# Kernel optimization log

Hardware: AMD Instinct MI355X
Metric: run time of the kernel (lower is better)

Reference implementation:

```python
import jax, jax.numpy as jnp
import numpy as np

B, NL, NT = 8, 64, 512   # graphs, ligand atoms/graph, target nodes/graph
CF = 128                 # per-node embedding dim (Linear(256,...) => 2*128)
H = 128                  # hidden_dim
K = 10                   # n_gaussians
E = 1024                 # ligand edges
BN_EPS = 1e-4


def setup_inputs() -> dict:
    key = jax.random.key(0)
    ks = jax.random.split(key, 24)
    inp = {}
    inp["h_l_x"] = jax.random.normal(ks[0], (B * NL, CF), jnp.float32)
    inp["h_t_x"] = jax.random.normal(ks[1], (B * NT, CF), jnp.float32)
    inp["h_l_pos"] = jax.random.normal(ks[2], (B * NL, 3), jnp.float32)
    inp["h_t_pos"] = jax.random.normal(ks[3], (B * NT, 3), jnp.float32)
    inp["edge_index"] = jax.random.randint(ks[4], (2, E), 0, B * NL, jnp.int64)
    s = 0.05
    inp["W1"] = jax.random.normal(ks[5], (2 * CF, H), jnp.float32) * s
    inp["b1"] = jnp.zeros((H,), jnp.float32)
    inp["gamma"] = jnp.ones((H,), jnp.float32)
    inp["beta"] = jnp.zeros((H,), jnp.float32)
    inp["rmean"] = jax.random.normal(ks[6], (H,), jnp.float32) * 0.1
    inp["rvar"] = jax.random.uniform(ks[7], (H,), jnp.float32, 0.5, 1.5)
    inp["Wpi"] = jax.random.normal(ks[8], (H, K), jnp.float32) * s
    inp["bpi"] = jnp.zeros((K,), jnp.float32)
    inp["Wsig"] = jax.random.normal(ks[9], (H, K), jnp.float32) * s
    inp["bsig"] = jnp.zeros((K,), jnp.float32)
    inp["Wmu"] = jax.random.normal(ks[10], (H, K), jnp.float32) * s
    inp["bmu"] = jnp.zeros((K,), jnp.float32)
    inp["Wat"] = jax.random.normal(ks[11], (CF, 28), jnp.float32) * s
    inp["bat"] = jnp.zeros((28,), jnp.float32)
    inp["Wbd"] = jax.random.normal(ks[12], (2 * CF, 6), jnp.float32) * s
    inp["bbd"] = jnp.zeros((6,), jnp.float32)
    return inp


def reference(h_l_x, h_t_x, h_l_pos, h_t_pos, edge_index,
              W1, b1, gamma, beta, rmean, rvar,
              Wpi, bpi, Wsig, bsig, Wmu, bmu, Wat, bat, Wbd, bbd):
    # dense batched node features (equal counts per graph => reshape)
    hl = h_l_x.reshape(B, NL, CF)
    ht = h_t_x.reshape(B, NT, CF)

    # cat([hl_repeat, ht_repeat]) @ W1 == hl@W1[:CF] + ht@W1[CF:] (broadcast add)
    zl = jnp.einsum('blc,ch->blh', hl, W1[:CF])          # [B,NL,H]
    zt = jnp.einsum('btc,ch->bth', ht, W1[CF:])          # [B,NT,H]
    z = zl[:, :, None, :] + zt[:, None, :, :] + b1       # [B,NL,NT,H]
    z = z.reshape(B * NL * NT, H)

    # BatchNorm1d (eval: running stats), ELU; Dropout is identity in eval
    z = (z - rmean) * (gamma / jnp.sqrt(rvar + BN_EPS)) + beta
    C = jax.nn.elu(z)

    pi = jax.nn.softmax(C @ Wpi + bpi, axis=-1)
    sigma = jax.nn.elu(C @ Wsig + bsig) + 1.1
    mu = jax.nn.elu(C @ Wmu + bmu) + 1.0

    # pairwise euclidean distances, detached in original
    pl = h_l_pos.reshape(B, NL, 3)
    pt = h_t_pos.reshape(B, NT, 3)
    d2 = (-2.0 * jnp.einsum('bld,btd->blt', pl, pt)
          + jnp.sum(pt ** 2, -1)[:, None, :]
          + jnp.sum(pl ** 2, -1)[:, :, None])
    dist = jnp.sqrt(d2).reshape(B * NL * NT)
    dist = jax.lax.stop_gradient(dist)[:, None]          # [P,1]

    atom_types = h_l_x @ Wat + bat                       # [B*NL,28]
    eb = jnp.concatenate([h_l_x[edge_index[0]], h_l_x[edge_index[1]]], axis=1)
    bond_types = eb @ Wbd + bbd                          # [E,6]

    C_batch = jnp.repeat(jnp.arange(B, dtype=jnp.int32), NL * NT)
    return (pi, sigma, mu, dist, atom_types, bond_types, C_batch)
```

## Files before the change

kernel.cpp:

```cpp
#include <hip/hip_runtime.h>
#include <hip/hip_bf16.h>
#include <cstdint>
#include <cstddef>

#define NB_B 8
#define NL   64
#define NT   512
#define CF   128
#define HD   128
#define NK   10
#define NE   1024

static constexpr size_t P_TOT    = (size_t)NB_B * NL * NT;
static constexpr size_t PI_OFF   = 0;
static constexpr size_t SIG_OFF  = P_TOT * 10;
static constexpr size_t MU_OFF   = SIG_OFF + P_TOT * 10;
static constexpr size_t DIST_OFF = MU_OFF + P_TOT * 10;
static constexpr size_t AT_OFF   = DIST_OFF + P_TOT;
static constexpr size_t BD_OFF   = AT_OFF + 512 * 28;
static constexpr size_t CB_OFF   = BD_OFF + NE * 6;

typedef __attribute__((ext_vector_type(8))) short short8;
typedef __attribute__((ext_vector_type(4))) float floatx4;
typedef __attribute__((ext_vector_type(2))) float floatx2;

union U8 { short8 s8; unsigned int u[4]; };

__device__ __forceinline__ float bf2f(unsigned short u) {
    return __uint_as_float(((unsigned int)u) << 16);
}
__device__ __forceinline__ unsigned short f2bf(float f) {
    unsigned int x = __float_as_uint(f);
    x = (x + 0x7FFFu + ((x >> 16) & 1u)) >> 16;
    return (unsigned short)x;
}
__device__ __forceinline__ unsigned int pk2bf(float a, float b) {
    __hip_bfloat162 h = __float22bfloat162_rn(make_float2(a, b));
    return *reinterpret_cast<unsigned int*>(&h);
}
__device__ __forceinline__ float elu(float x) {
    return fmaxf(x, 0.f) + (__expf(fminf(x, 0.f)) - 1.f);
}

__global__ __launch_bounds__(256) void k_pre(
    const float* __restrict__ hl,
    const float* __restrict__ ht,
    const float* __restrict__ W1,
    const float* __restrict__ b1,
    const float* __restrict__ gamma_,
    const float* __restrict__ beta_,
    const float* __restrict__ rmean,
    const float* __restrict__ rvar,
    const float* __restrict__ Wpi,
    const float* __restrict__ Wsig,
    const float* __restrict__ Wmu,
    unsigned short* __restrict__ zl,
    unsigned short* __restrict__ zt,
    unsigned short* __restrict__ wcomb_t)
{
    const int blk = blockIdx.x;
    const int tid = threadIdx.x;

    if (blk < 144) {
        const bool is_l = (blk < 16);
        const int rbase = is_l ? blk * 32 : (blk - 16) * 32;
        const float* A  = is_l ? hl : ht;
        const float* Wx = W1 + (is_l ? 0 : (size_t)CF * HD);
        unsigned short* Z = is_l ? zl : zt;

        const int wave = tid >> 6;
        const int lane = tid & 63;
        const int m    = lane & 15;
        const int kq   = (lane >> 4) * 8;
        const int n0   = wave * 32 + m;

        floatx4 acc[2][2];
        #pragma unroll
        for (int i = 0; i < 2; ++i)
            #pragma unroll
            for (int j = 0; j < 2; ++j)
                acc[i][j] = (floatx4){0.f, 0.f, 0.f, 0.f};

        #pragma unroll
        for (int kb = 0; kb < 4; ++kb) {
            const int k0 = kb * 32 + kq;
            short8 a[2];
            #pragma unroll
            for (int mt = 0; mt < 2; ++mt) {
                const float* ap = A + (size_t)(rbase + mt * 16 + m) * CF + k0;
                const float4 f0 = *(const float4*)ap;
                const float4 f1 = *(const float4*)(ap + 4);
                U8 t;
                t.u[0] = pk2bf(f0.x, f0.y);
                t.u[1] = pk2bf(f0.z, f0.w);
                t.u[2] = pk2bf(f1.x, f1.y);
                t.u[3] = pk2bf(f1.z, f1.w);
                a[mt] = t.s8;
            }
            short8 bf[2];
            #pragma unroll
            for (int nt = 0; nt < 2; ++nt) {
                const int n = n0 + nt * 16;
                float w[8];
                #pragma unroll
                for (int j = 0; j < 8; ++j)
                    w[j] = Wx[(size_t)(k0 + j) * HD + n];
                U8 t;
                #pragma unroll
                for (int j = 0; j < 4; ++j) t.u[j] = pk2bf(w[2*j], w[2*j+1]);
                bf[nt] = t.s8;
            }
            #pragma unroll
            for (int mt = 0; mt < 2; ++mt)
                #pragma unroll
                for (int nt = 0; nt < 2; ++nt)
                    acc[mt][nt] = __builtin_amdgcn_mfma_f32_16x16x32_bf16(a[mt], bf[nt], acc[mt][nt], 0, 0, 0);
        }

        #pragma unroll
        for (int nt = 0; nt < 2; ++nt) {
            const int col = n0 + nt * 16;
            const float s   = gamma_[col] * rsqrtf(rvar[col] + 1e-4f);
            const float off = is_l ? 0.f : ((b1[col] - rmean[col]) * s + beta_[col]);
            #pragma unroll
            for (int mt = 0; mt < 2; ++mt)
                #pragma unroll
                for (int r = 0; r < 4; ++r) {
                    const int row = rbase + mt * 16 + (lane >> 4) * 4 + r;
                    Z[(size_t)row * HD + col] = f2bf(acc[mt][nt][r] * s + off);
                }
        }
    } else {
        for (int i = tid; i < 32 * HD; i += 256) {
            const int n = i >> 7, k = i & 127;
            float v = 0.f;
            if (n < 10)      v = Wpi [k * NK + n];
            else if (n < 20) v = Wsig[k * NK + (n - 10)];
            else if (n < 30) v = Wmu [k * NK + (n - 20)];
            wcomb_t[i] = f2bf(v);
        }
    }
}

__global__ __launch_bounds__(256) void k_main(
    const unsigned short* __restrict__ zl,
    const unsigned short* __restrict__ zt,
    const unsigned short* __restrict__ wcomb_t,
    const float* __restrict__ bpi,
    const float* __restrict__ bsig,
    const float* __restrict__ bmu,
    const float* __restrict__ hlpos,
    const float* __restrict__ htpos,
    const float* __restrict__ hl,
    const int*   __restrict__ eidx,
    const float* __restrict__ Wat,
    const float* __restrict__ bat,
    const float* __restrict__ Wbd,
    const float* __restrict__ bbd,
    float* __restrict__ out)
{
    __shared__ float Dl[128 * 34];
    __shared__ float biass[32];
    __shared__ float pls[3];

    const int tid  = threadIdx.x;
    const int blk  = blockIdx.x;
    const int lane = tid & 63;
    const int wave = tid >> 6;
    const int m    = lane & 15;
    const int quad = lane >> 4;

    if (blk >= 2048) {
        const int ab = blk - 2048;
        if (ab < 4) {
            const int rbase = ab * 128 + wave * 32;
            floatx4 acc[2][2];
            #pragma unroll
            for (int i = 0; i < 2; ++i)
                #pragma unroll
                for (int j = 0; j < 2; ++j)
                    acc[i][j] = (floatx4){0.f, 0.f, 0.f, 0.f};
            #pragma unroll
            for (int kb = 0; kb < 4; ++kb) {
                const int k0 = kb * 32 + quad * 8;
                short8 a[2];
                #pragma unroll
                for (int mt = 0; mt < 2; ++mt) {
                    const float* ap = hl + (size_t)(rbase + mt * 16 + m) * CF + k0;
                    const float4 f0 = *(const float4*)ap;
                    const float4 f1 = *(const float4*)(ap + 4);
                    U8 t;
                    t.u[0] = pk2bf(f0.x, f0.y);
                    t.u[1] = pk2bf(f0.z, f0.w);
                    t.u[2] = pk2bf(f1.x, f1.y);
                    t.u[3] = pk2bf(f1.z, f1.w);
                    a[mt] = t.s8;
                }
                short8 bf[2];
                #pragma unroll
                for (int nt = 0; nt < 2; ++nt) {
                    const int n = nt * 16 + m;
                    const int nc = (n < 28) ? n : 0;
                    #pragma unroll
                    for (int j = 0; j < 8; ++j) {
                        const float w = Wat[(size_t)(k0 + j) * 28 + nc];
                        bf[nt][j] = (short)f2bf((n < 28) ? w : 0.f);
                    }
                }
                #pragma unroll
                for (int mt = 0; mt < 2; ++mt)
                    #pragma unroll
                    for (int nt = 0; nt < 2; ++nt)
                        acc[mt][nt] = __builtin_amdgcn_mfma_f32_16x16x32_bf16(a[mt], bf[nt], acc[mt][nt], 0, 0, 0);
            }
            #pragma unroll
            for (int nt = 0; nt < 2; ++nt) {
                const int col = nt * 16 + m;
                if (col < 28) {
                    const float bias = bat[col];
                    #pragma unroll
                    for (int mt = 0; mt < 2; ++mt)
                        #pragma unroll
                        for (int r = 0; r < 4; ++r) {
                            const int row = rbase + mt * 16 + quad * 4 + r;
                            out[AT_OFF + (size_t)row * 28 + col] = acc[mt][nt][r] + bias;
                        }
                }
            }
        } else {
            const int rbase = (ab - 4) * 128 + wave * 32;
            const int e0 = rbase + m, e1 = rbase + 16 + m;
            const int s00 = eidx[e0], s01 = eidx[NE + e0];
            const int s10 = eidx[e1], s11 = eidx[NE + e1];
            floatx4 acc[2];
            acc[0] = (floatx4){0.f, 0.f, 0.f, 0.f};
            acc[1] = (floatx4){0.f, 0.f, 0.f, 0.f};
            const int nc = (m < 6) ? m : 0;
            #pragma unroll
            for (int kb = 0; kb < 8; ++kb) {
                const int k0 = kb * 32 + quad * 8;
                const bool lo = (k0 < 128);
                const int off = lo ? k0 : (k0 - 128);
                short8 a[2];
                #pragma unroll
                for (int mt = 0; mt < 2; ++mt) {
                    const int src = lo ? (mt ? s10 : s00) : (mt ? s11 : s01);
                    const float* ap = hl + (size_t)src * CF + off;
                    const float4 f0 = *(const float4*)ap;
                    const float4 f1 = *(const float4*)(ap + 4);
                    U8 t;
                    t.u[0] = pk2bf(f0.x, f0.y);
                    t.u[1] = pk2bf(f0.z, f0.w);
                    t.u[2] = pk2bf(f1.x, f1.y);
                    t.u[3] = pk2bf(f1.z, f1.w);
                    a[mt] = t.s8;
                }
                short8 bf;
                #pragma unroll
                for (int j = 0; j < 8; ++j) {
                    const float w = Wbd[(size_t)(k0 + j) * 6 + nc];
                    bf[j] = (short)f2bf((m < 6) ? w : 0.f);
                }
                acc[0] = __builtin_amdgcn_mfma_f32_16x16x32_bf16(a[0], bf, acc[0], 0, 0, 0);
                acc[1] = __builtin_amdgcn_mfma_f32_16x16x32_bf16(a[1], bf, acc[1], 0, 0, 0);
            }
            if (m < 6) {
                const float bias = bbd[m];
                #pragma unroll
                for (int mt = 0; mt < 2; ++mt)
                    #pragma unroll
                    for (int r = 0; r < 4; ++r) {
                        const int row = rbase + mt * 16 + quad * 4 + r;
                        out[BD_OFF + (size_t)row * 6 + m] = acc[mt][r] + bias;
                    }
            }
        }
        return;
    }

    const int b  = blk >> 8;
    const int l  = (blk >> 2) & 63;
    const int ch = blk & 3;

    if (tid < 32) {
        float v = 0.f;
        if (tid < 10)      v = bpi[tid];
        else if (tid < 20) v = bsig[tid - 10];
        else if (tid < 30) v = bmu[tid - 20];
        biass[tid] = v;
    } else if (tid < 35) {
        pls[tid - 32] = hlpos[(size_t)(b * NL + l) * 3 + (tid - 32)];
    }

    short8 bfrag[2][4];
    #pragma unroll
    for (int nt = 0; nt < 2; ++nt)
        #pragma unroll
        for (int kb = 0; kb < 4; ++kb)
            bfrag[nt][kb] = *(const short8*)(wcomb_t + (size_t)(nt * 16 + m) * HD + kb * 32 + quad * 8);

    const unsigned short* zlr = zl + (size_t)(b * NL + l) * HD;
    const unsigned short* ztb = zt + (size_t)(b * NT + ch * 128) * HD;

    floatx4 acc[2][2];
    #pragma unroll
    for (int i = 0; i < 2; ++i)
        #pragma unroll
        for (int j = 0; j < 2; ++j)
            acc[i][j] = (floatx4){0.f, 0.f, 0.f, 0.f};

    #pragma unroll
    for (int kb = 0; kb < 4; ++kb) {
        const int k0 = kb * 32 + quad * 8;
        const short8 zlv = *(const short8*)(zlr + k0);
        float zf[8];
        #pragma unroll
        for (int j = 0; j < 8; ++j) zf[j] = bf2f((unsigned short)zlv[j]);

        short8 a[2];
        #pragma unroll
        for (int mt = 0; mt < 2; ++mt) {
            const int row = wave * 32 + mt * 16 + m;
            const short8 ztv = *(const short8*)(ztb + (size_t)row * HD + k0);
            float e[8];
            #pragma unroll
            for (int j = 0; j < 8; ++j)
                e[j] = elu(zf[j] + bf2f((unsigned short)ztv[j]));
            U8 t;
            #pragma unroll
            for (int j = 0; j < 4; ++j) t.u[j] = pk2bf(e[2*j], e[2*j+1]);
            a[mt] = t.s8;
        }
        #pragma unroll
        for (int mt = 0; mt < 2; ++mt)
            #pragma unroll
            for (int nt = 0; nt < 2; ++nt)
                acc[mt][nt] = __builtin_amdgcn_mfma_f32_16x16x32_bf16(a[mt], bfrag[nt][kb], acc[mt][nt], 0, 0, 0);
    }

    #pragma unroll
    for (int mt = 0; mt < 2; ++mt)
        #pragma unroll
        for (int nt = 0; nt < 2; ++nt)
            #pragma unroll
            for (int r = 0; r < 4; ++r) {
                const int row = wave * 32 + mt * 16 + quad * 4 + r;
                const int col = nt * 16 + m;
                Dl[row * 34 + col] = acc[mt][nt][r];
            }
    __syncthreads();

    const size_t gp = ((size_t)(b * NL + l)) * NT + ch * 128 + (tid & 127);
    if (tid < 128) {
        const int p = tid;
        float v[10];
        float mx = -1e30f;
        #pragma unroll
        for (int n = 0; n < 10; ++n) {
            v[n] = Dl[p * 34 + n] + biass[n];
            mx = fmaxf(mx, v[n]);
        }
        float s = 0.f;
        #pragma unroll
        for (int n = 0; n < 10; ++n) { v[n] = __expf(v[n] - mx); s += v[n]; }
        const float inv = 1.f / s;
        floatx2* po = (floatx2*)(out + PI_OFF + gp * 10);
        #pragma unroll
        for (int n = 0; n < 5; ++n) po[n] = (floatx2){v[2*n] * inv, v[2*n+1] * inv};
    } else {
        const int p = tid - 128;
        float sg[10], mv[10];
        #pragma unroll
        for (int n = 0; n < 10; ++n) {
            sg[n] = elu(Dl[p * 34 + 10 + n] + biass[10 + n]) + 1.1f;
            mv[n] = elu(Dl[p * 34 + 20 + n] + biass[20 + n]) + 1.0f;
        }
        floatx2* ps = (floatx2*)(out + SIG_OFF + gp * 10);
        floatx2* pm = (floatx2*)(out + MU_OFF  + gp * 10);
        #pragma unroll
        for (int n = 0; n < 5; ++n) {
            ps[n] = (floatx2){sg[2*n], sg[2*n+1]};
            pm[n] = (floatx2){mv[2*n], mv[2*n+1]};
        }
        const int t = ch * 128 + p;
        const size_t pb = (size_t)(b * NT + t) * 3;
        const float dx = pls[0] - htpos[pb + 0];
        const float dy = pls[1] - htpos[pb + 1];
        const float dz = pls[2] - htpos[pb + 2];
        out[DIST_OFF + gp] = sqrtf(dx * dx + dy * dy + dz * dz);
        out[CB_OFF + gp]   = (float)b;
    }
}

extern "C" void kernel_launch(void* const* d_in, const int* in_sizes, int n_in,
                              void* d_out, int out_size, void* d_ws, size_t ws_size,
                              hipStream_t stream)
{
    const float* hl     = (const float*)d_in[0];
    const float* ht     = (const float*)d_in[1];
    const float* hlpos  = (const float*)d_in[2];
    const float* htpos  = (const float*)d_in[3];
    const int*   eidx   = (const int*)d_in[4];
    const float* W1     = (const float*)d_in[5];
    const float* b1     = (const float*)d_in[6];
    const float* gamma_ = (const float*)d_in[7];
    const float* beta_  = (const float*)d_in[8];
    const float* rmean  = (const float*)d_in[9];
    const float* rvar   = (const float*)d_in[10];
    const float* Wpi    = (const float*)d_in[11];
    const float* bpi    = (const float*)d_in[12];
    const float* Wsig   = (const float*)d_in[13];
    const float* bsig   = (const float*)d_in[14];
    const float* Wmu    = (const float*)d_in[15];
    const float* bmu    = (const float*)d_in[16];
    const float* Wat    = (const float*)d_in[17];
    const float* bat    = (const float*)d_in[18];
    const float* Wbd    = (const float*)d_in[19];
    const float* bbd    = (const float*)d_in[20];

    float* out = (float*)d_out;
    unsigned short* ws  = (unsigned short*)d_ws;
    unsigned short* zl      = ws;
    unsigned short* zt      = ws + 512 * 128;
    unsigned short* wcomb_t = ws + 512 * 128 + 4096 * 128;

    k_pre<<<145, 256, 0, stream>>>(hl, ht, W1, b1, gamma_, beta_, rmean, rvar,
                                   Wpi, Wsig, Wmu, zl, zt, wcomb_t);
    k_main<<<2060, 256, 0, stream>>>(zl, zt, wcomb_t, bpi, bsig, bmu, hlpos, htpos,
                                     hl, eidx, Wat, bat, Wbd, bbd, out);
}
```

Baseline: 132.3 us.

## Fuse pre and main kernels into one persistent kernel with grid barrier

Merges the projection kernel and the main pairwise kernel into one launch of 1024 blocks. The blocks first compute zl/zt (now 16-row tiles over 288 blocks), meet at an atomic-counter grid barrier, then each block loops over two work units of the former main grid. The aim is to remove the second kernel launch and the gap between the two kernels. In exchange it adds a memset and a spin barrier. The barrier deadlocks unless all 1024 blocks are resident at once, which depends on occupancy (launch_bounds 256,4).

```diff
diff --git a/kernel.cpp b/kernel.cpp
--- a/kernel.cpp
+++ b/kernel.cpp
@@ -10,6 +10,7 @@
 #define HD   128
 #define NK   10
 #define NE   1024
+#define NBLK 1024u
 
 static constexpr size_t P_TOT    = (size_t)NB_B * NL * NT;
 static constexpr size_t PI_OFF   = 0;
@@ -42,9 +43,12 @@
     return fmaxf(x, 0.f) + (__expf(fminf(x, 0.f)) - 1.f);
 }
 
-__global__ __launch_bounds__(256) void k_pre(
+__global__ __launch_bounds__(256, 4) void k_all(
     const float* __restrict__ hl,
     const float* __restrict__ ht,
+    const float* __restrict__ hlpos,
+    const float* __restrict__ htpos,
+    const int*   __restrict__ eidx,
     const float* __restrict__ W1,
     const float* __restrict__ b1,
     const float* __restrict__ gamma_,
@@ -52,51 +56,57 @@
     const float* __restrict__ rmean,
     const float* __restrict__ rvar,
     const float* __restrict__ Wpi,
+    const float* __restrict__ bpi,
     const float* __restrict__ Wsig,
+    const float* __restrict__ bsig,
     const float* __restrict__ Wmu,
+    const float* __restrict__ bmu,
+    const float* __restrict__ Wat,
+    const float* __restrict__ bat,
+    const float* __restrict__ Wbd,
+    const float* __restrict__ bbd,
     unsigned short* __restrict__ zl,
     unsigned short* __restrict__ zt,
-    unsigned short* __restrict__ wcomb_t)
+    unsigned short* __restrict__ wcomb_t,
+    unsigned int*   __restrict__ cnt,
+    float* __restrict__ out)
 {
-    const int blk = blockIdx.x;
-    const int tid = threadIdx.x;
-
-    if (blk < 144) {
-        const bool is_l = (blk < 16);
-        const int rbase = is_l ? blk * 32 : (blk - 16) * 32;
+    __shared__ float Dl[128 * 34];
+    __shared__ float biass[32];
+    __shared__ float pls[3];
+
+    const int blk0 = blockIdx.x;
+    const int tid  = threadIdx.x;
+    const int lane = tid & 63;
+    const int wave = tid >> 6;
+    const int m    = lane & 15;
+    const int quad = lane >> 4;
+
+    if (blk0 < 288) {
+        const bool is_l = (blk0 < 32);
+        const int rbase = is_l ? blk0 * 16 : (blk0 - 32) * 16;
         const float* A  = is_l ? hl : ht;
         const float* Wx = W1 + (is_l ? 0 : (size_t)CF * HD);
         unsigned short* Z = is_l ? zl : zt;
-
-        const int wave = tid >> 6;
-        const int lane = tid & 63;
-        const int m    = lane & 15;
-        const int kq   = (lane >> 4) * 8;
-        const int n0   = wave * 32 + m;
-
-        floatx4 acc[2][2];
-        #pragma unroll
-        for (int i = 0; i < 2; ++i)
-            #pragma unroll
-            for (int j = 0; j < 2; ++j)
-                acc[i][j] = (floatx4){0.f, 0.f, 0.f, 0.f};
+        const int n0 = wave * 32 + m;
+
+        floatx4 acc[2];
+        acc[0] = (floatx4){0.f, 0.f, 0.f, 0.f};
+        acc[1] = (floatx4){0.f, 0.f, 0.f, 0.f};
 
         #pragma unroll
         for (int kb = 0; kb < 4; ++kb) {
-            const int k0 = kb * 32 + kq;
-            short8 a[2];
-            #pragma unroll
-            for (int mt = 0; mt < 2; ++mt) {
-                const float* ap = A + (size_t)(rbase + mt * 16 + m) * CF + k0;
-                const float4 f0 = *(const float4*)ap;
-                const float4 f1 = *(const float4*)(ap + 4);
-                U8 t;
-                t.u[0] = pk2bf(f0.x, f0.y);
-                t.u[1] = pk2bf(f0.z, f0.w);
-                t.u[2] = pk2bf(f1.x, f1.y);
-                t.u[3] = pk2bf(f1.z, f1.w);
-                a[mt] = t.s8;
-            }
+            const int k0 = kb * 32 + quad * 8;
+            const float* ap = A + (size_t)(rbase + m) * CF + k0;
+            const float4 f0 = *(const float4*)ap;
+            const float4 f1 = *(const float4*)(ap + 4);
+            U8 t;
+            t.u[0] = pk2bf(f0.x, f0.y);
+            t.u[1] = pk2bf(f0.z, f0.w);
+            t.u[2] = pk2bf(f1.x, f1.y);
+            t.u[3] = pk2bf(f1.z, f1.w);
+            const short8 a = t.s8;
+
             short8 bf[2];
             #pragma unroll
             for (int nt = 0; nt < 2; ++nt) {
@@ -105,16 +115,14 @@
                 #pragma unroll
                 for (int j = 0; j < 8; ++j)
                     w[j] = Wx[(size_t)(k0 + j) * HD + n];
-                U8 t;
-                #pragma unroll
-                for (int j = 0; j < 4; ++j) t.u[j] = pk2bf(w[2*j], w[2*j+1]);
-                bf[nt] = t.s8;
-            }
-            #pragma unroll
-            for (int mt = 0; mt < 2; ++mt)
-                #pragma unroll
-                for (int nt = 0; nt < 2; ++nt)
-                    acc[mt][nt] = __builtin_amdgcn_mfma_f32_16x16x32_bf16(a[mt], bf[nt], acc[mt][nt], 0, 0, 0);
+                U8 tt;
+                #pragma unroll
+                for (int j = 0; j < 4; ++j) tt.u[j] = pk2bf(w[2*j], w[2*j+1]);
+                bf[nt] = tt.s8;
+            }
+            #pragma unroll
+            for (int nt = 0; nt < 2; ++nt)
+                acc[nt] = __builtin_amdgcn_mfma_f32_16x16x32_bf16(a, bf[nt], acc[nt], 0, 0, 0);
         }
 
         #pragma unroll
@@ -123,14 +131,12 @@
             const float s   = gamma_[col] * rsqrtf(rvar[col] + 1e-4f);
             const float off = is_l ? 0.f : ((b1[col] - rmean[col]) * s + beta_[col]);
             #pragma unroll
-            for (int mt = 0; mt < 2; ++mt)
-                #pragma unroll
-                for (int r = 0; r < 4; ++r) {
-                    const int row = rbase + mt * 16 + (lane >> 4) * 4 + r;
-                    Z[(size_t)row * HD + col] = f2bf(acc[mt][nt][r] * s + off);
-                }
-        }
-    } else {
+            for (int r = 0; r < 4; ++r) {
+                const int row = rbase + quad * 4 + r;
+                Z[(size_t)row * HD + col] = f2bf(acc[nt][r] * s + off);
+            }
+        }
+    } else if (blk0 == 288) {
         for (int i = tid; i < 32 * HD; i += 256) {
             const int n = i >> 7, k = i & 127;
             float v = 0.f;
@@ -140,255 +146,243 @@
             wcomb_t[i] = f2bf(v);
         }
     }
-}
-
-__global__ __launch_bounds__(256) void k_main(
-    const unsigned short* __restrict__ zl,
-    const unsigned short* __restrict__ zt,
-    const unsigned short* __restrict__ wcomb_t,
-    const float* __restrict__ bpi,
-    const float* __restrict__ bsig,
-    const float* __restrict__ bmu,
-    const float* __restrict__ hlpos,
-    const float* __restrict__ htpos,
-    const float* __restrict__ hl,
-    const int*   __restrict__ eidx,
-    const float* __restrict__ Wat,
-    const float* __restrict__ bat,
-    const float* __restrict__ Wbd,
-    const float* __restrict__ bbd,
-    float* __restrict__ out)
-{
-    __shared__ float Dl[128 * 34];
-    __shared__ float biass[32];
-    __shared__ float pls[3];
-
-    const int tid  = threadIdx.x;
-    const int blk  = blockIdx.x;
-    const int lane = tid & 63;
-    const int wave = tid >> 6;
-    const int m    = lane & 15;
-    const int quad = lane >> 4;
-
-    if (blk >= 2048) {
-        const int ab = blk - 2048;
-        if (ab < 4) {
-            const int rbase = ab * 128 + wave * 32;
-            floatx4 acc[2][2];
-            #pragma unroll
-            for (int i = 0; i < 2; ++i)
-                #pragma unroll
-                for (int j = 0; j < 2; ++j)
-                    acc[i][j] = (floatx4){0.f, 0.f, 0.f, 0.f};
-            #pragma unroll
-            for (int kb = 0; kb < 4; ++kb) {
-                const int k0 = kb * 32 + quad * 8;
-                short8 a[2];
-                #pragma unroll
-                for (int mt = 0; mt < 2; ++mt) {
-                    const float* ap = hl + (size_t)(rbase + mt * 16 + m) * CF + k0;
-                    const float4 f0 = *(const float4*)ap;
-                    const float4 f1 = *(const float4*)(ap + 4);
-                    U8 t;
-                    t.u[0] = pk2bf(f0.x, f0.y);
-                    t.u[1] = pk2bf(f0.z, f0.w);
-                    t.u[2] = pk2bf(f1.x, f1.y);
-                    t.u[3] = pk2bf(f1.z, f1.w);
-                    a[mt] = t.s8;
+
+    __threadfence();
+    __syncthreads();
+    if (tid == 0) {
+        __hip_atomic_fetch_add(cnt, 1u, __ATOMIC_ACQ_REL, __HIP_MEMORY_SCOPE_AGENT);
+        unsigned int v;
+        do {
+            v = __hip_atomic_load(cnt, __ATOMIC_ACQUIRE, __HIP_MEMORY_SCOPE_AGENT);
+            if (v >= NBLK) break;
+            __builtin_amdgcn_s_sleep(2);
+        } while (true);
+    }
+    __syncthreads();
+    __threadfence();
+
+    for (int u = blk0; u < 2060; u += 1024) {
+        if (u >= 2048) {
+            const int ab = u - 2048;
+            if (ab < 4) {
+                const int rbase = ab * 128 + wave * 32;
+                floatx4 acc[2][2];
+                #pragma unroll
+                for (int i = 0; i < 2; ++i)
+                    #pragma unroll
+                    for (int j = 0; j < 2; ++j)
+                        acc[i][j] = (floatx4){0.f, 0.f, 0.f, 0.f};
+                #pragma unroll
+                for (int kb = 0; kb < 4; ++kb) {
+                    const int k0 = kb * 32 + quad * 8;
+                    short8 a[2];
+                    #pragma unroll
+                    for (int mt = 0; mt < 2; ++mt) {
+                        const float* ap = hl + (size_t)(rbase + mt * 16 + m) * CF + k0;
+                        const float4 f0 = *(const float4*)ap;
+                        const float4 f1 = *(const float4*)(ap + 4);
+                        U8 t;
+                        t.u[0] = pk2bf(f0.x, f0.y);
+                        t.u[1] = pk2bf(f0.z, f0.w);
+                        t.u[2] = pk2bf(f1.x, f1.y);
+                        t.u[3] = pk2bf(f1.z, f1.w);
+                        a[mt] = t.s8;
+                    }
+                    short8 bf[2];
+                    #pragma unroll
+                    for (int nt = 0; nt < 2; ++nt) {
+                        const int n = nt * 16 + m;
+                        const int nc = (n < 28) ? n : 0;
+                        #pragma unroll
+                        for (int j = 0; j < 8; ++j) {
+                            const float w = Wat[(size_t)(k0 + j) * 28 + nc];
+                            bf[nt][j] = (short)f2bf((n < 28) ? w : 0.f);
+                        }
+                    }
+                    #pragma unroll
+                    for (int mt = 0; mt < 2; ++mt)
+                        #pragma unroll
+                        for (int nt = 0; nt < 2; ++nt)
+                            acc[mt][nt] = __builtin_amdgcn_mfma_f32_16x16x32_bf16(a[mt], bf[nt], acc[mt][nt], 0, 0, 0);
                 }
-                short8 bf[2];
                 #pragma unroll
                 for (int nt = 0; nt < 2; ++nt) {
-                    const int n = nt * 16 + m;
-                    const int nc = (n < 28) ? n : 0;
-                    #pragma unroll
-                    for (int j = 0; j < 8; ++j) {
-                        const float w = Wat[(size_t)(k0 + j) * 28 + nc];
-                        bf[nt][j] = (short)f2bf((n < 28) ? w : 0.f);
+                    const int col = nt * 16 + m;
+                    if (col < 28) {
+                        const float bias = bat[col];
+                        #pragma unroll
+                        for (int mt = 0; mt < 2; ++mt)
+                            #pragma unroll
+                            for (int r = 0; r < 4; ++r) {
+                                const int row = rbase + mt * 16 + quad * 4 + r;
+                                out[AT_OFF + (size_t)row * 28 + col] = acc[mt][nt][r] + bias;
+                            }
                     }
                 }
-                #pragma unroll
-                for (int mt = 0; mt < 2; ++mt)
-                    #pragma unroll
-                    for (int nt = 0; nt < 2; ++nt)
-                        acc[mt][nt] = __builtin_amdgcn_mfma_f32_16x16x32_bf16(a[mt], bf[nt], acc[mt][nt], 0, 0, 0);
-            }
-            #pragma unroll
-            for (int nt = 0; nt < 2; ++nt) {
-                const int col = nt * 16 + m;
-                if (col < 28) {
-                    const float bias = bat[col];
+            } else {
+                const int rbase = (ab - 4) * 128 + wave * 32;
+                const int e0 = rbase + m, e1 = rbase + 16 + m;
+                const int s00 = eidx[e0], s01 = eidx[NE + e0];
+                const int s10 = eidx[e1], s11 = eidx[NE + e1];
+                floatx4 acc[2];
+                acc[0] = (floatx4){0.f, 0.f, 0.f, 0.f};
+                acc[1] = (floatx4){0.f, 0.f, 0.f, 0.f};
+                const int nc = (m < 6) ? m : 0;
+                #pragma unroll
+                for (int kb = 0; kb < 8; ++kb) {
+                    const int k0 = kb * 32 + quad * 8;
+                    const bool lo = (k0 < 128);
+                    const int off = lo ? k0 : (k0 - 128);
+                    short8 a[2];
+                    #pragma unroll
+                    for (int mt = 0; mt < 2; ++mt) {
+                        const int src = lo ? (mt ? s10 : s00) : (mt ? s11 : s01);
+                        const float* ap = hl + (size_t)src * CF + off;
+                        const float4 f0 = *(const float4*)ap;
+                        const float4 f1 = *(const float4*)(ap + 4);
+                        U8 t;
+                        t.u[0] = pk2bf(f0.x, f0.y);
+                        t.u[1] = pk2bf(f0.z, f0.w);
+                        t.u[2] = pk2bf(f1.x, f1.y);
+                        t.u[3] = pk2bf(f1.z, f1.w);
+                        a[mt] = t.s8;
+                    }
+                    short8 bf;
+                    #pragma unroll
+                    for (int j = 0; j < 8; ++j) {
+                        const float w = Wbd[(size_t)(k0 + j) * 6 + nc];
+                        bf[j] = (short)f2bf((m < 6) ? w : 0.f);
+                    }
+                    acc[0] = __builtin_amdgcn_mfma_f32_16x16x32_bf16(a[0], bf, acc[0], 0, 0, 0);
+                    acc[1] = __builtin_amdgcn_mfma_f32_16x16x32_bf16(a[1], bf, acc[1], 0, 0, 0);
+                }
+                if (m < 6) {
+                    const float bias = bbd[m];
                     #pragma unroll
                     for (int mt = 0; mt < 2; ++mt)
                         #pragma unroll
                         for (int r = 0; r < 4; ++r) {
                             const int row = rbase + mt * 16 + quad * 4 + r;
-                            out[AT_OFF + (size_t)row * 28 + col] = acc[mt][nt][r] + bias;
+                            out[BD_OFF + (size_t)row * 6 + m] = acc[mt][r] + bias;
                         }
                 }
             }
+            continue;
+        }
+
+        const int b  = u >> 8;
+        const int l  = (u >> 2) & 63;
+        const int ch = u & 3;
+
+        if (tid < 32) {
+            float v = 0.f;
+            if (tid < 10)      v = bpi[tid];
+            else if (tid < 20) v = bsig[tid - 10];
+            else if (tid < 30) v = bmu[tid - 20];
+            biass[tid] = v;
+        } else if (tid < 35) {
+            pls[tid - 32] = hlpos[(size_t)(b * NL + l) * 3 + (tid - 32)];
+        }
+
+        short8 bfrag[2][4];
+        #pragma unroll
+        for (int nt = 0; nt < 2; ++nt)
+            #pragma unroll
+            for (int kb = 0; kb < 4; ++kb)
+                bfrag[nt][kb] = *(const short8*)(wcomb_t + (size_t)(nt * 16 + m) * HD + kb * 32 + quad * 8);
+
+        const unsigned short* zlr = zl + (size_t)(b * NL + l) * HD;
+        const unsigned short* ztb = zt + (size_t)(b * NT + ch * 128) * HD;
+
+        floatx4 acc[2][2];
+        #pragma unroll
+        for (int i = 0; i < 2; ++i)
+            #pragma unroll
+            for (int j = 0; j < 2; ++j)
+                acc[i][j] = (floatx4){0.f, 0.f, 0.f, 0.f};
+
+        #pragma unroll
+        for (int kb = 0; kb < 4; ++kb) {
+            const int k0 = kb * 32 + quad * 8;
+            const short8 zlv = *(const short8*)(zlr + k0);
+            float zf[8];
+            #pragma unroll
+            for (int j = 0; j < 8; ++j) zf[j] = bf2f((unsigned short)zlv[j]);
+
+            short8 a[2];
+            #pragma unroll
+            for (int mt = 0; mt < 2; ++mt) {
+                const int row = wave * 32 + mt * 16 + m;
+                const short8 ztv = *(const short8*)(ztb + (size_t)row * HD + k0);
+                float e[8];
+                #pragma unroll
+                for (int j = 0; j < 8; ++j)
+                    e[j] = elu(zf[j] + bf2f((unsigned short)ztv[j]));
+                U8 t;
+                #pragma unroll
+                for (int j = 0; j < 4; ++j) t.u[j] = pk2bf(e[2*j], e[2*j+1]);
+                a[mt] = t.s8;
+            }
+            #pragma unroll
+            for (int mt = 0; mt < 2; ++mt)
+                #pragma unroll
+                for (int nt = 0; nt < 2; ++nt)
+                    acc[mt][nt] = __builtin_amdgcn_mfma_f32_16x16x32_bf16(a[mt], bfrag[nt][kb], acc[mt][nt], 0, 0, 0);
+        }
+
+        #pragma unroll
+        for (int mt = 0; mt < 2; ++mt)
+            #pragma unroll
+            for (int nt = 0; nt < 2; ++nt)
+                #pragma unroll
+                for (int r = 0; r < 4; ++r) {
+                    const int row = wave * 32 + mt * 16 + quad * 4 + r;
+                    const int col = nt * 16 + m;
+                    Dl[row * 34 + col] = acc[mt][nt][r];
+                }
+        __syncthreads();
+
+        const size_t gp = ((size_t)(b * NL + l)) * NT + ch * 128 + (tid & 127);
+        if (tid < 128) {
+            const int p = tid;
+            float v[10];
+            float mx = -1e30f;
+            #pragma unroll
+            for (int n = 0; n < 10; ++n) {
+                v[n] = Dl[p * 34 + n] + biass[n];
+                mx = fmaxf(mx, v[n]);
+            }
+            float s = 0.f;
+            #pragma unroll
+            for (int n = 0; n < 10; ++n) { v[n] = __expf(v[n] - mx); s += v[n]; }
+            const float inv = 1.f / s;
+            floatx2* po = (floatx2*)(out + PI_OFF + gp * 10);
+            #pragma unroll
+            for (int n = 0; n < 5; ++n) po[n] = (floatx2){v[2*n] * inv, v[2*n+1] * inv};
         } else {
-            const int rbase = (ab - 4) * 128 + wave * 32;
-            const int e0 = rbase + m, e1 = rbase + 16 + m;
-            const int s00 = eidx[e0], s01 = eidx[NE + e0];
-            const int s10 = eidx[e1], s11 = eidx[NE + e1];
-            floatx4 acc[2];
-            acc[0] = (floatx4){0.f, 0.f, 0.f, 0.f};
-            acc[1] = (floatx4){0.f, 0.f, 0.f, 0.f};
-            const int nc = (m < 6) ? m : 0;
-            #pragma unroll
-            for (int kb = 0; kb < 8; ++kb) {
-                const int k0 = kb * 32 + quad * 8;
-                const bool lo = (k0 < 128);
-                const int off = lo ? k0 : (k0 - 128);
-                short8 a[2];
-                #pragma unroll
-                for (int mt = 0; mt < 2; ++mt) {
-                    const int src = lo ? (mt ? s10 : s00) : (mt ? s11 : s01);
-                    const float* ap = hl + (size_t)src * CF + off;
-                    const float4 f0 = *(const float4*)ap;
-                    const float4 f1 = *(const float4*)(ap + 4);
-                    U8 t;
-                    t.u[0] = pk2bf(f0.x, f0.y);
-                    t.u[1] = pk2bf(f0.z, f0.w);
-                    t.u[2] = pk2bf(f1.x, f1.y);
-                    t.u[3] = pk2bf(f1.z, f1.w);
-                    a[mt] = t.s8;
-                }
-                short8 bf;
-                #pragma unroll
-                for (int j = 0; j < 8; ++j) {
-                    const float w = Wbd[(size_t)(k0 + j) * 6 + nc];
-                    bf[j] = (short)f2bf((m < 6) ? w : 0.f);
-                }
-                acc[0] = __builtin_amdgcn_mfma_f32_16x16x32_bf16(a[0], bf, acc[0], 0, 0, 0);
-                acc[1] = __builtin_amdgcn_mfma_f32_16x16x32_bf16(a[1], bf, acc[1], 0, 0, 0);
-            }
-            if (m < 6) {
-                const float bias = bbd[m];
-                #pragma unroll
-                for (int mt = 0; mt < 2; ++mt)
-                    #pragma unroll
-                    for (int r = 0; r < 4; ++r) {
-                        const int row = rbase + mt * 16 + quad * 4 + r;
-                        out[BD_OFF + (size_t)row * 6 + m] = acc[mt][r] + bias;
-                    }
-            }
-        }
-        return;
-    }
-
-    const int b  = blk >> 8;
-    const int l  = (blk >> 2) & 63;
-    const int ch = blk & 3;
-
-    if (tid < 32) {
-        float v = 0.f;
-        if (tid < 10)      v = bpi[tid];
-        else if (tid < 20) v = bsig[tid - 10];
-        else if (tid < 30) v = bmu[tid - 20];
-        biass[tid] = v;
-    } else if (tid < 35) {
-        pls[tid - 32] = hlpos[(size_t)(b * NL + l) * 3 + (tid - 32)];
-    }
-
-    short8 bfrag[2][4];
-    #pragma unroll
-    for (int nt = 0; nt < 2; ++nt)
-        #pragma unroll
-        for (int kb = 0; kb < 4; ++kb)
-            bfrag[nt][kb] = *(const short8*)(wcomb_t + (size_t)(nt * 16 + m) * HD + kb * 32 + quad * 8);
-
-    const unsigned short* zlr = zl + (size_t)(b * NL + l) * HD;
-    const unsigned short* ztb = zt + (size_t)(b * NT + ch * 128) * HD;
-
-    floatx4 acc[2][2];
-    #pragma unroll
-    for (int i = 0; i < 2; ++i)
-        #pragma unroll
-        for (int j = 0; j < 2; ++j)
-            acc[i][j] = (floatx4){0.f, 0.f, 0.f, 0.f};
-
-    #pragma unroll
-    for (int kb = 0; kb < 4; ++kb) {
-        const int k0 = kb * 32 + quad * 8;
-        const short8 zlv = *(const short8*)(zlr + k0);
-        float zf[8];
-        #pragma unroll
-        for (int j = 0; j < 8; ++j) zf[j] = bf2f((unsigned short)zlv[j]);
-
-        short8 a[2];
-        #pragma unroll
-        for (int mt = 0; mt < 2; ++mt) {
-            const int row = wave * 32 + mt * 16 + m;
-            const short8 ztv = *(const short8*)(ztb + (size_t)row * HD + k0);
-            float e[8];
-            #pragma unroll
-            for (int j = 0; j < 8; ++j)
-                e[j] = elu(zf[j] + bf2f((unsigned short)ztv[j]));
-            U8 t;
-            #pragma unroll
-            for (int j = 0; j < 4; ++j) t.u[j] = pk2bf(e[2*j], e[2*j+1]);
-            a[mt] = t.s8;
-        }
-        #pragma unroll
-        for (int mt = 0; mt < 2; ++mt)
-            #pragma unroll
-            for (int nt = 0; nt < 2; ++nt)
-                acc[mt][nt] = __builtin_amdgcn_mfma_f32_16x16x32_bf16(a[mt], bfrag[nt][kb], acc[mt][nt], 0, 0, 0);
-    }
-
-    #pragma unroll
-    for (int mt = 0; mt < 2; ++mt)
-        #pragma unroll
-        for (int nt = 0; nt < 2; ++nt)
-            #pragma unroll
-            for (int r = 0; r < 4; ++r) {
-                const int row = wave * 32 + mt * 16 + quad * 4 + r;
-                const int col = nt * 16 + m;
-                Dl[row * 34 + col] = acc[mt][nt][r];
-            }
-    __syncthreads();
-
-    const size_t gp = ((size_t)(b * NL + l)) * NT + ch * 128 + (tid & 127);
-    if (tid < 128) {
-        const int p = tid;
-        float v[10];
-        float mx = -1e30f;
-        #pragma unroll
-        for (int n = 0; n < 10; ++n) {
-            v[n] = Dl[p * 34 + n] + biass[n];
-            mx = fmaxf(mx, v[n]);
-        }
-        float s = 0.f;
-        #pragma unroll
-        for (int n = 0; n < 10; ++n) { v[n] = __expf(v[n] - mx); s += v[n]; }
-        const float inv = 1.f / s;
-        floatx2* po = (floatx2*)(out + PI_OFF + gp * 10);
-        #pragma unroll
-        for (int n = 0; n < 5; ++n) po[n] = (floatx2){v[2*n] * inv, v[2*n+1] * inv};
-    } else {
-        const int p = tid - 128;
-        float sg[10], mv[10];
-        #pragma unroll
-        for (int n = 0; n < 10; ++n) {
-            sg[n] = elu(Dl[p * 34 + 10 + n] + biass[10 + n]) + 1.1f;
-            mv[n] = elu(Dl[p * 34 + 20 + n] + biass[20 + n]) + 1.0f;
-        }
-        floatx2* ps = (floatx2*)(out + SIG_OFF + gp * 10);
-        floatx2* pm = (floatx2*)(out + MU_OFF  + gp * 10);
-        #pragma unroll
-        for (int n = 0; n < 5; ++n) {
-            ps[n] = (floatx2){sg[2*n], sg[2*n+1]};
-            pm[n] = (floatx2){mv[2*n], mv[2*n+1]};
-        }
-        const int t = ch * 128 + p;
-        const size_t pb = (size_t)(b * NT + t) * 3;
-        const float dx = pls[0] - htpos[pb + 0];
-        const float dy = pls[1] - htpos[pb + 1];
-        const float dz = pls[2] - htpos[pb + 2];
-        out[DIST_OFF + gp] = sqrtf(dx * dx + dy * dy + dz * dz);
-        out[CB_OFF + gp]   = (float)b;
+            const int p = tid - 128;
+            float sg[10], mv[10];
+            #pragma unroll
+            for (int n = 0; n < 10; ++n) {
+                sg[n] = elu(Dl[p * 34 + 10 + n] + biass[10 + n]) + 1.1f;
+                mv[n] = elu(Dl[p * 34 + 20 + n] + biass[20 + n]) + 1.0f;
+            }
+            floatx2* ps = (floatx2*)(out + SIG_OFF + gp * 10);
+            floatx2* pm = (floatx2*)(out + MU_OFF  + gp * 10);
+            #pragma unroll
+            for (int n = 0; n < 5; ++n) {
+                ps[n] = (floatx2){sg[2*n], sg[2*n+1]};
+                pm[n] = (floatx2){mv[2*n], mv[2*n+1]};
+            }
+            const int t = ch * 128 + p;
+            const size_t pb = (size_t)(b * NT + t) * 3;
+            const float dx = pls[0] - htpos[pb + 0];
+            const float dy = pls[1] - htpos[pb + 1];
+            const float dz = pls[2] - htpos[pb + 2];
+            out[DIST_OFF + gp] = sqrtf(dx * dx + dy * dy + dz * dz);
+            out[CB_OFF + gp]   = (float)b;
+        }
+        __syncthreads();
     }
 }
 
@@ -419,13 +413,16 @@
     const float* bbd    = (const float*)d_in[20];
 
     float* out = (float*)d_out;
-    unsigned short* ws  = (unsigned short*)d_ws;
-    unsigned short* zl      = ws;
-    unsigned short* zt      = ws + 512 * 128;
-    unsigned short* wcomb_t = ws + 512 * 128 + 4096 * 128;
-
-    k_pre<<<145, 256, 0, stream>>>(hl, ht, W1, b1, gamma_, beta_, rmean, rvar,
-                                   Wpi, Wsig, Wmu, zl, zt, wcomb_t);
-    k_main<<<2060, 256, 0, stream>>>(zl, zt, wcomb_t, bpi, bsig, bmu, hlpos, htpos,
-                                     hl, eidx, Wat, bat, Wbd, bbd, out);
-}
+    unsigned char* wsb  = (unsigned char*)d_ws;
+    unsigned short* zl      = (unsigned short*)wsb;
+    unsigned short* zt      = (unsigned short*)(wsb + 131072);
+    unsigned short* wcomb_t = (unsigned short*)(wsb + 1179648);
+    unsigned int*   cnt     = (unsigned int*)  (wsb + 1187840);
+
+    hipMemsetAsync(cnt, 0, 4, stream);
+    k_all<<<1024, 256, 0, stream>>>(hl, ht, hlpos, htpos, eidx,
+                                    W1, b1, gamma_, beta_, rmean, rvar,
+                                    Wpi, bpi, Wsig, bsig, Wmu, bmu,
+                                    Wat, bat, Wbd, bbd,
+                                    zl, zt, wcomb_t, cnt, out);
+}
```

Measured after the change: 487.2 us. 268% more time.
